# Optimization experiments

Measured on AMD Instinct MI355X. Metric: run time of the kernel, lower is better.

## Reference

```python
import jax, jax.numpy as jnp
import numpy as np

N = 33554432  # number of elements
POS_WEIGHT = 1.0
NEG_WEIGHT = 8.0
EPS = 1e-07


def setup_inputs() -> dict:
    key = jax.random.key(0)
    k1, k2 = jax.random.split(key)
    outputs = jax.random.uniform(k1, (N,), dtype=jnp.float32)  # probabilities in (0,1)
    targets = jax.random.randint(k2, (N,), 0, 2, dtype=jnp.int32)  # binary labels
    return {"outputs": outputs, "targets": targets}


def reference(outputs, targets):
    # weight-select, log, and mean-reduction in one fused elementwise pass
    pos = POS_WEIGHT * -jnp.log(outputs + EPS)
    neg = NEG_WEIGHT * -jnp.log(1.0 - outputs + EPS)
    loss = jnp.where(targets == 1, pos, neg)
    return jnp.mean(loss)
```

## Files before the change

### kernel.cpp

```cpp
#include <hip/hip_runtime.h>

#define NEG_W 8.0f
#define EPS 1e-7f
#define TPB 256
#define VPT 4
#define BLOCKS 8192

typedef float f32x4 __attribute__((ext_vector_type(4)));
typedef int   i32x4 __attribute__((ext_vector_type(4)));

__global__ __launch_bounds__(TPB) void bce_partial(
    const f32x4* __restrict__ out4, const i32x4* __restrict__ tgt4,
    float* __restrict__ partials) {
  const int base = blockIdx.x * (TPB * VPT) + threadIdx.x;

  f32x4 o0 = out4[base + 0 * TPB];
  f32x4 o1 = out4[base + 1 * TPB];
  f32x4 o2 = out4[base + 2 * TPB];
  f32x4 o3 = out4[base + 3 * TPB];
  i32x4 t0 = tgt4[base + 0 * TPB];
  i32x4 t1 = tgt4[base + 1 * TPB];
  i32x4 t2 = tgt4[base + 2 * TPB];
  i32x4 t3 = tgt4[base + 3 * TPB];
  asm volatile("" : "+v"(o0), "+v"(o1), "+v"(o2), "+v"(o3),
                    "+v"(t0), "+v"(t1), "+v"(t2), "+v"(t3));

  float acc0 = 0.0f, acc1 = 0.0f, acc2 = 0.0f, acc3 = 0.0f;
#define BCE_BODY(o, t)                                              \
  {                                                                 \
    float x0 = (t.x == 1) ? (o.x + EPS) : (1.0f - o.x + EPS);       \
    float w0 = (t.x == 1) ? 1.0f : NEG_W;                           \
    float x1 = (t.y == 1) ? (o.y + EPS) : (1.0f - o.y + EPS);       \
    float w1 = (t.y == 1) ? 1.0f : NEG_W;                           \
    float x2 = (t.z == 1) ? (o.z + EPS) : (1.0f - o.z + EPS);       \
    float w2 = (t.z == 1) ? 1.0f : NEG_W;                           \
    float x3 = (t.w == 1) ? (o.w + EPS) : (1.0f - o.w + EPS);       \
    float w3 = (t.w == 1) ? 1.0f : NEG_W;                           \
    acc0 = fmaf(w0, __logf(x0), acc0);                              \
    acc1 = fmaf(w1, __logf(x1), acc1);                              \
    acc2 = fmaf(w2, __logf(x2), acc2);                              \
    acc3 = fmaf(w3, __logf(x3), acc3);                              \
  }
  BCE_BODY(o0, t0)
  BCE_BODY(o1, t1)
  BCE_BODY(o2, t2)
  BCE_BODY(o3, t3)
#undef BCE_BODY

  float sum = -((acc0 + acc1) + (acc2 + acc3));

  for (int off = 32; off > 0; off >>= 1)
    sum += __shfl_down(sum, off, 64);

  __shared__ float wsum[TPB / 64];
  const int lane = threadIdx.x & 63;
  const int wid = threadIdx.x >> 6;
  if (lane == 0) wsum[wid] = sum;
  __syncthreads();
  if (threadIdx.x == 0) {
    float s = 0.0f;
    for (int w = 0; w < TPB / 64; ++w) s += wsum[w];
    partials[blockIdx.x] = s;
  }
}

__global__ __launch_bounds__(TPB) void bce_finalize(
    const float* __restrict__ partials, float* __restrict__ out, int nblocks,
    double inv_n) {
  double s = 0.0;
  for (int i = threadIdx.x; i < nblocks; i += TPB) s += (double)partials[i];
  for (int off = 32; off > 0; off >>= 1)
    s += __shfl_down(s, off, 64);
  __shared__ double wsum[TPB / 64];
  const int lane = threadIdx.x & 63;
  const int wid = threadIdx.x >> 6;
  if (lane == 0) wsum[wid] = s;
  __syncthreads();
  if (threadIdx.x == 0) {
    double tot = 0.0;
    for (int w = 0; w < TPB / 64; ++w) tot += wsum[w];
    out[0] = (float)(tot * inv_n);
  }
}

extern "C" void kernel_launch(void* const* d_in, const int* in_sizes, int n_in,
                              void* d_out, int out_size, void* d_ws, size_t ws_size,
                              hipStream_t stream) {
  const f32x4* out4 = (const f32x4*)d_in[0];
  const i32x4* tgt4 = (const i32x4*)d_in[1];
  const int n = in_sizes[0];
  float* partials = (float*)d_ws;
  (void)n;

  bce_partial<<<BLOCKS, TPB, 0, stream>>>(out4, tgt4, partials);
  bce_finalize<<<1, TPB, 0, stream>>>(partials, (float*)d_out, BLOCKS,
                                      1.0 / (double)33554432);
}
```

Before: 280.1 us.

## Switch to grid-strided persistent blocks with double-buffered software-pipelined loads

Cuts the grid from 8192 to 2048 blocks, so each thread now walks 16 float4/int4 chunks with a grid-wide stride instead of 4 contiguous ones. The loop double-buffers two pairs of loads, issuing the next pair before computing the current one. The aim is to keep more memory requests in flight per wave and to hide load latency behind the log math, and it also shrinks the partials array the finalize kernel reduces. The cost is more live vector registers per thread and a loop with fewer blocks to hide latency across.

```diff
diff --git a/kernel.cpp b/kernel.cpp
--- a/kernel.cpp
+++ b/kernel.cpp
@@ -3,8 +3,9 @@
 #define NEG_W 8.0f
 #define EPS 1e-7f
 #define TPB 256
-#define VPT 4
-#define BLOCKS 8192
+#define BLOCKS 2048
+#define STRIDE (BLOCKS * TPB)
+#define SUBT 8
 
 typedef float f32x4 __attribute__((ext_vector_type(4)));
 typedef int   i32x4 __attribute__((ext_vector_type(4)));
@@ -12,20 +13,10 @@
 __global__ __launch_bounds__(TPB) void bce_partial(
     const f32x4* __restrict__ out4, const i32x4* __restrict__ tgt4,
     float* __restrict__ partials) {
-  const int base = blockIdx.x * (TPB * VPT) + threadIdx.x;
-
-  f32x4 o0 = out4[base + 0 * TPB];
-  f32x4 o1 = out4[base + 1 * TPB];
-  f32x4 o2 = out4[base + 2 * TPB];
-  f32x4 o3 = out4[base + 3 * TPB];
-  i32x4 t0 = tgt4[base + 0 * TPB];
-  i32x4 t1 = tgt4[base + 1 * TPB];
-  i32x4 t2 = tgt4[base + 2 * TPB];
-  i32x4 t3 = tgt4[base + 3 * TPB];
-  asm volatile("" : "+v"(o0), "+v"(o1), "+v"(o2), "+v"(o3),
-                    "+v"(t0), "+v"(t1), "+v"(t2), "+v"(t3));
+  const int tid = blockIdx.x * TPB + threadIdx.x;
 
   float acc0 = 0.0f, acc1 = 0.0f, acc2 = 0.0f, acc3 = 0.0f;
+
 #define BCE_BODY(o, t)                                              \
   {                                                                 \
     float x0 = (t.x == 1) ? (o.x + EPS) : (1.0f - o.x + EPS);       \
@@ -41,10 +32,30 @@
     acc2 = fmaf(w2, __logf(x2), acc2);                              \
     acc3 = fmaf(w3, __logf(x3), acc3);                              \
   }
-  BCE_BODY(o0, t0)
-  BCE_BODY(o1, t1)
-  BCE_BODY(o2, t2)
-  BCE_BODY(o3, t3)
+
+  int p = tid;
+  f32x4 oa0 = out4[p], oa1 = out4[p + STRIDE];
+  i32x4 ta0 = tgt4[p], ta1 = tgt4[p + STRIDE];
+
+#pragma unroll 1
+  for (int s = 0; s < SUBT; s += 2) {
+    const int pb = p + 2 * STRIDE;
+    f32x4 ob0 = out4[pb], ob1 = out4[pb + STRIDE];
+    i32x4 tb0 = tgt4[pb], tb1 = tgt4[pb + STRIDE];
+
+    BCE_BODY(oa0, ta0)
+    BCE_BODY(oa1, ta1)
+
+    const int pa = p + 4 * STRIDE;
+    if (s + 2 < SUBT) {
+      oa0 = out4[pa];  oa1 = out4[pa + STRIDE];
+      ta0 = tgt4[pa];  ta1 = tgt4[pa + STRIDE];
+    }
+
+    BCE_BODY(ob0, tb0)
+    BCE_BODY(ob1, tb1)
+    p = pa;
+  }
 #undef BCE_BODY
 
   float sum = -((acc0 + acc1) + (acc2 + acc3));
```

Result: no change. 280.9 us (+0.3%).
